# Kernel optimization log

Measured on AMD Instinct MI355X. Metric: run time of the kernel, lower is better.

## Reference

```python
import jax, jax.numpy as jnp
import numpy as np

C = 256        # channels
HEADS = 4
D = C // HEADS # per-head dim
M = 3          # num modalities
EPS = 1e-5
NEG_SLOPE = 0.2  # PyG GATv2 leaky_relu slope


def setup_inputs() -> dict:
    key = jax.random.key(0)
    ks = iter(jax.random.split(key, 40))
    def nrm(shape, s=0.02):
        return jax.random.normal(next(ks), shape, dtype=jnp.float32) * s
    B, H, W = 2, 128, 128
    inp = {}
    for m in range(M):
        inp[f"modal{m}"] = jax.random.normal(next(ks), (B, C, H, W), dtype=jnp.float32)
    # fusion node initializer MLP: Linear-ReLU-Linear
    inp["fn_w1"] = nrm((C, C)); inp["fn_b1"] = jnp.zeros((C,), jnp.float32)
    inp["fn_w2"] = nrm((C, C)); inp["fn_b2"] = jnp.zeros((C,), jnp.float32)
    # two GATv2 layers + layernorms
    for l in range(2):
        inp[f"l{l}_wl"] = nrm((C, C)); inp[f"l{l}_bl"] = jnp.zeros((C,), jnp.float32)
        inp[f"l{l}_wr"] = nrm((C, C)); inp[f"l{l}_br"] = jnp.zeros((C,), jnp.float32)
        inp[f"l{l}_att"] = nrm((HEADS, D), 0.1)
        inp[f"l{l}_bias"] = jnp.zeros((C,), jnp.float32)
        inp[f"ln{l}_g"] = jnp.ones((C,), jnp.float32)
        inp[f"ln{l}_b"] = jnp.zeros((C,), jnp.float32)
    # spatial interaction: conv3x3 (no bias) + BN (eval mode) + ReLU
    inp["conv_w"] = nrm((C, C, 3, 3))
    inp["bn_g"] = jnp.ones((C,), jnp.float32); inp["bn_b"] = jnp.zeros((C,), jnp.float32)
    inp["bn_m"] = jnp.zeros((C,), jnp.float32); inp["bn_v"] = jnp.ones((C,), jnp.float32)
    return inp


def _gatv2(x, wl, bl, wr, br, att, bias):
    # Dense batched GATv2 over P tiny complete graphs (self-loops included,
    # matching PyG GATv2Conv add_self_loops=True default).
    P, N, Cc = x.shape
    xl = (x @ wl + bl).reshape(P, N, HEADS, D)  # source / message features
    xr = (x @ wr + br).reshape(P, N, HEADS, D)  # target features
    e = jax.nn.leaky_relu(xr[:, :, None] + xl[:, None, :], NEG_SLOPE)  # [P,Ni,Nj,H,D]
    scores = jnp.einsum('pijhd,hd->pijh', e, att)
    alpha = jax.nn.softmax(scores, axis=2)  # softmax over source nodes j per target i
    out = jnp.einsum('pijh,pjhd->pihd', alpha, xl)
    return out.reshape(P, N, Cc) + bias


def _layernorm(x, g, b):
    mu = jnp.mean(x, axis=-1, keepdims=True)
    var = jnp.mean((x - mu) ** 2, axis=-1, keepdims=True)
    return (x - mu) * jax.lax.rsqrt(var + EPS) * g + b


def _forward(modal0, modal1, modal2, fn_w1, fn_b1, fn_w2, fn_b2,
             l0_wl, l0_bl, l0_wr, l0_br, l0_att, l0_bias, ln0_g, ln0_b,
             l1_wl, l1_bl, l1_wr, l1_br, l1_att, l1_bias, ln1_g, ln1_b,
             conv_w, bn_g, bn_b, bn_m, bn_v):
    B, _, H, W = modal0.shape
    stacked = jnp.stack([modal0, modal1, modal2], axis=1)        # [B,M,C,H,W]
    modal_nodes = stacked.transpose(0, 3, 4, 1, 2).reshape(-1, M, C)  # [P,M,C]
    mean_feat = jnp.mean(modal_nodes, axis=1, keepdims=True)     # [P,1,C]
    fusion = jax.nn.relu(mean_feat @ fn_w1 + fn_b1) @ fn_w2 + fn_b2
    x = jnp.concatenate([fusion, modal_nodes], axis=1)           # [P,M+1,C]
    for (wl, bl, wr, br, att, bias, g, b) in (
        (l0_wl, l0_bl, l0_wr, l0_br, l0_att, l0_bias, ln0_g, ln0_b),
        (l1_wl, l1_bl, l1_wr, l1_br, l1_att, l1_bias, ln1_g, ln1_b),
    ):
        x = _layernorm(_gatv2(x, wl, bl, wr, br, att, bias) + x, g, b)
    fused = x[:, 0, :].reshape(B, H, W, C).transpose(0, 3, 1, 2)  # [B,C,H,W]
    y = jax.lax.conv_general_dilated(
        fused, conv_w, window_strides=(1, 1), padding='SAME',
        dimension_numbers=('NCHW', 'OIHW', 'NCHW'))
    bc = lambda v: v[None, :, None, None]
    y = (y - bc(bn_m)) * bc(jax.lax.rsqrt(bn_v + EPS)) * bc(bn_g) + bc(bn_b)
    y = jax.nn.relu(y)
    return y + fused


def reference(modal0, modal1, modal2, fn_w1, fn_b1, fn_w2, fn_b2,
              l0_wl, l0_bl, l0_wr, l0_br, l0_att, l0_bias, ln0_g, ln0_b,
              l1_wl, l1_bl, l1_wr, l1_br, l1_att, l1_bias, ln1_g, ln1_b,
              conv_w, bn_g, bn_b, bn_m, bn_v):
    return _forward(modal0, modal1, modal2, fn_w1, fn_b1, fn_w2, fn_b2,
                    l0_wl, l0_bl, l0_wr, l0_br, l0_att, l0_bias, ln0_g, ln0_b,
                    l1_wl, l1_bl, l1_wr, l1_br, l1_att, l1_bias, ln1_g, ln1_b,
                    conv_w, bn_g, bn_b, bn_m, bn_v)
```

## Files before the change

kernel.cpp:

```cpp
#include <hip/hip_runtime.h>


#define Pn 32768
#define PADR 16900

typedef __attribute__((ext_vector_type(8))) short bf16x8;
typedef __attribute__((ext_vector_type(4))) float f32x4;
typedef __attribute__((ext_vector_type(4))) unsigned short u16x4;
typedef __attribute__((ext_vector_type(8))) unsigned short u16x8;
typedef __attribute__((ext_vector_type(2))) unsigned int u32x2;

__device__ __forceinline__ float b2f(short s) {
  unsigned u = ((unsigned)(unsigned short)s) << 16;
  float f;
  __builtin_memcpy(&f, &u, 4);
  return f;
}
__device__ __forceinline__ float asf(unsigned u) {
  float f;
  __builtin_memcpy(&f, &u, 4);
  return f;
}
__device__ __forceinline__ short f2b(float f) {
  unsigned u;
  __builtin_memcpy(&u, &f, 4);
  u += 0x7fffu + ((u >> 16) & 1u);
  return (short)(u >> 16);
}
__device__ __forceinline__ float ldany(const void* p, int i, int bf) {
  return bf ? b2f(((const short*)p)[i]) : ((const float*)p)[i];
}
__device__ __forceinline__ void gload_lds16(const short* g, short* l) {
  __builtin_amdgcn_global_load_lds(
      (const __attribute__((address_space(1))) unsigned int*)g,
      (__attribute__((address_space(3))) unsigned int*)l, 16, 0, 0);
}

__device__ __forceinline__ int xcd_swz(int bid, int nwg) {
  int q = nwg >> 3, r = nwg & 7;
  int x = bid & 7, p = bid >> 3;
  return (x < r ? x * (q + 1) : r * (q + 1) + (x - r) * q) + p;
}

template <int CTRL>
__device__ __forceinline__ float dpp_add(float v) {
  int s;
  __builtin_memcpy(&s, &v, 4);
  int m = __builtin_amdgcn_update_dpp(0, s, CTRL, 0xF, 0xF, false);
  float f;
  __builtin_memcpy(&f, &m, 4);
  return v + f;
}
__device__ __forceinline__ float rsum16(float v) {
  v = dpp_add<0x121>(v);
  v = dpp_add<0x122>(v);
  v = dpp_add<0x124>(v);
  v = dpp_add<0x128>(v);
  return v;
}

__global__ __launch_bounds__(256) void detect_dtype(const void* probe, int* flag) {
  const short* s = (const short*)probe;
  int cnt = 0;
#pragma unroll
  for (int i = 0; i < 8; ++i) {
    short v = s[(threadIdx.x * 8 + i) * 2];
    int e = ((unsigned short)v >> 7) & 0xFF;
    cnt += (e >= 100 && e <= 127) ? 1 : 0;
  }
  __shared__ int tot;
  if (threadIdx.x == 0) tot = 0;
  __syncthreads();
  atomicAdd(&tot, cnt);
  __syncthreads();
  if (threadIdx.x == 0) flag[0] = (tot > 1024) ? 1 : 0;
}

struct P18 { const void* p[18]; };
__global__ __launch_bounds__(256) void prep_params(P18 s, const int* flag, float* pb) {
  int bf = *flag;
  int t = threadIdx.x;
#pragma unroll
  for (int v = 0; v < 18; ++v) pb[v * 256 + t] = ldany(s.p[v], t, bf);
}

__global__ __launch_bounds__(256) void prep_gemm_w(
    const void* w0, const void* w1, const void* w2, const void* w3,
    const void* w4, const void* w5, const int* flag, short* wt) {
  int bf = *flag;
  const void* src;
  switch (blockIdx.y) {
    case 0: src = w0; break;
    case 1: src = w1; break;
    case 2: src = w2; break;
    case 3: src = w3; break;
    case 4: src = w4; break;
    default: src = w5; break;
  }
  int idx = blockIdx.x * 256 + threadIdx.x;
  int ntile = idx >> 12;
  int kt = (idx >> 9) & 7;
  int l = (idx >> 3) & 63;
  int j = idx & 7;
  int r = l & 15, q = l >> 4;
  int n = ntile * 16 + r;
  int k = kt * 32 + q * 8 + j;
  wt[blockIdx.y * 65536 + idx] = f2b(ldany(src, k * 256 + n, bf));
}

__global__ __launch_bounds__(256) void prep_conv_w(const void* cw, const int* flag,
                                                   short* cwt) {
  int bf = *flag;
  int idx = blockIdx.x * 256 + threadIdx.x;
  int tap = idx >> 16;
  int n = (idx >> 8) & 255;
  int k = idx & 255;
  cwt[idx] = f2b(ldany(cw, (n * 256 + k) * 9 + tap, bf));
}

__global__ __launch_bounds__(256) void zero_border(short* rowsPad) {
  int id = blockIdx.x;
  int b = id >= 516;
  int r = id - b * 516;
  int hp, wp;
  if (r < 130)      { hp = 0;       wp = r; }
  else if (r < 260) { hp = 129;     wp = r - 130; }
  else if (r < 388) { hp = r - 259; wp = 0; }
  else              { hp = r - 387; wp = 129; }
  rowsPad[(b * PADR + hp * 130 + wp) * 256 + threadIdx.x] = 0;
}

__global__ __launch_bounds__(256) void gather_chunk(
    const void* m0, const void* m1, const void* m2, const int* flag,
    short* Xc, short* meanc, int sb0) {
  const int bf = *flag;
  const int bx = blockIdx.x;
  const int seg = bx >> 2;
  const int cb = (bx & 3) * 64;
  const int sb = sb0 + seg;
  const int wt = sb & 1, h = (sb >> 1) & 127, b = sb >> 8;
  const int w0 = wt * 64;
  const int lp0 = seg * 64;
  const int t = threadIdx.x;

  __shared__ short tile[3][64][72];
  const void* srcs[3] = {m0, m1, m2};

  const int lsub = t & 7;
#pragma unroll
  for (int pass = 0; pass < 2; ++pass) {
    int c_l = pass * 32 + (t >> 3);
    long long gbase = ((long long)(b * 256 + cb + c_l) * 128 + h) * 128 + w0 + lsub * 8;
#pragma unroll
    for (int m = 0; m < 3; ++m) {
      u16x8 v;
      if (bf) {
        v = *(const u16x8*)((const short*)srcs[m] + gbase);
      } else {
        const float* gp = (const float*)srcs[m] + gbase;
        f32x4 f0 = *(const f32x4*)gp;
        f32x4 f1 = *(const f32x4*)(gp + 4);
#pragma unroll
        for (int k = 0; k < 4; ++k) {
          v[k] = (unsigned short)f2b(f0[k]);
          v[4 + k] = (unsigned short)f2b(f1[k]);
        }
      }
      *(u16x8*)&tile[m][c_l][lsub * 8] = v;
    }
  }
  __syncthreads();

  const int c0 = (t & 7) * 8;
#pragma unroll
  for (int pass = 0; pass < 2; ++pass) {
    int w_l = pass * 32 + (t >> 3);
    float mv[8];
#pragma unroll
    for (int m = 0; m < 3; ++m) {
      u16x8 v;
#pragma unroll
      for (int k = 0; k < 8; ++k) {
        short s = tile[m][c0 + k][w_l];
        v[k] = (unsigned short)s;
        float f = b2f(s);
        mv[k] = (m == 0) ? f : mv[k] + f;
      }
      *(u16x8*)(Xc + (long long)((lp0 + w_l) * 4 + 1 + m) * 256 + cb + c0) = v;
    }
    u16x8 mb;
#pragma unroll
    for (int k = 0; k < 8; ++k)
      mb[k] = (unsigned short)f2b(mv[k] * (1.f / 3.f));
    *(u16x8*)(meanc + (long long)(lp0 + w_l) * 256 + cb + c0) = mb;
  }
}

template <int RELU>
__global__ __launch_bounds__(256, 3) void gemm_tile(
    const short* __restrict__ A, const short* __restrict__ Bf,
    const float* __restrict__ bias, short* __restrict__ out, int ostride) {
  __shared__ short lds[2][4096];
  const int t = threadIdx.x;
  const int l = t & 63, wv = t >> 6;
  const int bid = blockIdx.y * gridDim.x + blockIdx.x;
  const int wg = xcd_swz(bid, gridDim.x * gridDim.y);
  const int n0 = (wg % gridDim.x) * 128;
  const int m0 = (wg / gridDim.x) * 128;
  const int r = l & 15, q = l >> 4;
  const int wm = wv & 1, wn = wv >> 1;

  const short* Bw = Bf + (((n0 >> 4) + wn * 4) << 12) + l * 8;

  f32x4 acc[4][4];
#pragma unroll
  for (int a = 0; a < 4; ++a)
#pragma unroll
    for (int c = 0; c < 4; ++c) acc[a][c] = (f32x4){0.f, 0.f, 0.f, 0.f};

  auto stage = [&](int kt, int bufi) {
    const int k0 = kt * 32;
#pragma unroll
    for (int j = 0; j < 2; ++j) {
      int s0 = j * 256 + wv * 64;
      int row = (s0 + l) >> 2;
      int chs = (l & 3) ^ ((row >> 1) & 3);
      gload_lds16(A + (m0 + row) * 256 + k0 + chs * 8, &lds[bufi][s0 * 8]);
    }
  };

  stage(0, 0);
  __syncthreads();
#pragma unroll
  for (int kt = 0; kt < 8; ++kt) {
    const int cur = kt & 1;
    bf16x8 bfr[4], af[4];
#pragma unroll
    for (int c = 0; c < 4; ++c)
      bfr[c] = *(const bf16x8*)(Bw + (c * 8 + kt) * 512);
#pragma unroll
    for (int a = 0; a < 4; ++a) {
      int R = wm * 64 + a * 16 + r;
      int ch = q ^ ((R >> 1) & 3);
      af[a] = *(const bf16x8*)(&lds[cur][R * 32 + ch * 8]);
    }
    if (kt < 7) stage(kt + 1, cur ^ 1);
#pragma unroll
    for (int a = 0; a < 4; ++a)
#pragma unroll
      for (int c = 0; c < 4; ++c)
        acc[a][c] = __builtin_amdgcn_mfma_f32_16x16x32_bf16(
            af[a], bfr[c], acc[a][c], 0, 0, 0);
    if (kt < 7) __syncthreads();
  }

#pragma unroll
  for (int c = 0; c < 4; ++c) {
    int n = n0 + wn * 64 + c * 16 + r;
    float bs = bias[n];
#pragma unroll
    for (int a = 0; a < 4; ++a)
#pragma unroll
      for (int i = 0; i < 4; ++i) {
        int m = m0 + wm * 64 + a * 16 + q * 4 + i;
        float v = acc[a][c][i] + bs;
        if (RELU) v = fmaxf(v, 0.f);
        out[m * ostride + n] = f2b(v);
      }
  }
}

__global__ __launch_bounds__(256) void attn_ln(
    const short* __restrict__ XLRc,
    const float* __restrict__ att, const float* __restrict__ bias,
    const float* __restrict__ lng, const float* __restrict__ lnb,
    short* __restrict__ Xc, int pOff, short* rowsPad, short* fimgb,
    int writeFused) {
  const int lane = threadIdx.x & 63;
  const int wv = threadIdx.x >> 6;
  const int e = lane & 15;
  const int lp = blockIdx.x * 16 + wv * 4 + (lane >> 4);
  const int pg = pOff + lp;

  float out[4][4][4];
#pragma unroll
  for (int h = 0; h < 4; ++h) {
    float av[4];
#pragma unroll
    for (int k = 0; k < 4; ++k) av[k] = att[h * 64 + e * 4 + k];
    float xlf[4][4], xrf[4][4];
#pragma unroll
    for (int j = 0; j < 4; ++j) {
      const short* rb = XLRc + (lp * 4 + j) * 512 + h * 64 + e * 4;
      u32x2 xl2 = *(const u32x2*)rb;
      u32x2 xr2 = *(const u32x2*)(rb + 256);
      xlf[j][0] = asf(xl2[0] << 16); xlf[j][1] = asf(xl2[0] & 0xffff0000u);
      xlf[j][2] = asf(xl2[1] << 16); xlf[j][3] = asf(xl2[1] & 0xffff0000u);
      xrf[j][0] = asf(xr2[0] << 16); xrf[j][1] = asf(xr2[0] & 0xffff0000u);
      xrf[j][2] = asf(xr2[1] << 16); xrf[j][3] = asf(xr2[1] & 0xffff0000u);
    }
    float rp[4], lp_[4];
#pragma unroll
    for (int j = 0; j < 4; ++j) {
      float r = 0.f, l2 = 0.f;
#pragma unroll
      for (int k = 0; k < 4; ++k) {
        r += xrf[j][k] * av[k];
        l2 += xlf[j][k] * av[k];
      }
      rp[j] = r;
      lp_[j] = l2;
    }
#pragma unroll
    for (int i = 0; i < 4; ++i) {
      float s[4];
#pragma unroll
      for (int j = 0; j < 4; ++j) {
        float acc = 0.f;
#pragma unroll
        for (int k = 0; k < 4; ++k) {
          float t = xrf[i][k] + xlf[j][k];
          acc += __builtin_fabsf(t) * av[k];
        }
        float ap = 0.6f * (rp[i] + lp_[j]) + 0.4f * acc;
        s[j] = rsum16(ap);
      }
      float mx = fmaxf(fmaxf(s[0], s[1]), fmaxf(s[2], s[3]));
      float e0 = __expf(s[0] - mx), e1 = __expf(s[1] - mx);
      float e2 = __expf(s[2] - mx), e3 = __expf(s[3] - mx);
      float inv = __builtin_amdgcn_rcpf(e0 + e1 + e2 + e3);
      float a0 = e0 * inv, a1 = e1 * inv, a2 = e2 * inv, a3 = e3 * inv;
#pragma unroll
      for (int k = 0; k < 4; ++k)
        out[i][h][k] =
            a0 * xlf[0][k] + a1 * xlf[1][k] + a2 * xlf[2][k] + a3 * xlf[3][k];
    }
  }

  float biasf[4][4];
#pragma unroll
  for (int h = 0; h < 4; ++h)
#pragma unroll
    for (int k = 0; k < 4; ++k) biasf[h][k] = bias[h * 64 + e * 4 + k];

#pragma unroll
  for (int i = 0; i < 4; ++i) {
    float y[4][4], sm = 0.f;
#pragma unroll
    for (int h = 0; h < 4; ++h) {
      u32x2 rv2 = *(const u32x2*)(Xc + (lp * 4 + i) * 256 + h * 64 + e * 4);
      float r0 = asf(rv2[0] << 16), r1 = asf(rv2[0] & 0xffff0000u);
      float r2 = asf(rv2[1] << 16), r3 = asf(rv2[1] & 0xffff0000u);
      y[h][0] = out[i][h][0] + biasf[h][0] + r0;
      y[h][1] = out[i][h][1] + biasf[h][1] + r1;
      y[h][2] = out[i][h][2] + biasf[h][2] + r2;
      y[h][3] = out[i][h][3] + biasf[h][3] + r3;
      sm += y[h][0] + y[h][1] + y[h][2] + y[h][3];
    }
    sm = rsum16(sm);
    float mu = sm * (1.f / 256.f);
    float vs = 0.f;
#pragma unroll
    for (int h = 0; h < 4; ++h)
#pragma unroll
      for (int k = 0; k < 4; ++k) {
        float d = y[h][k] - mu;
        vs += d * d;
      }
    vs = rsum16(vs);
    float rs = rsqrtf(vs * (1.f / 256.f) + 1e-5f);
#pragma unroll
    for (int h = 0; h < 4; ++h) {
      float g0 = lng[h * 64 + e * 4 + 0], g1 = lng[h * 64 + e * 4 + 1];
      float g2 = lng[h * 64 + e * 4 + 2], g3 = lng[h * 64 + e * 4 + 3];
      float b0 = lnb[h * 64 + e * 4 + 0], b1 = lnb[h * 64 + e * 4 + 1];
      float b2 = lnb[h * 64 + e * 4 + 2], b3 = lnb[h * 64 + e * 4 + 3];
      u16x4 ov;
      ov[0] = (unsigned short)f2b((y[h][0] - mu) * rs * g0 + b0);
      ov[1] = (unsigned short)f2b((y[h][1] - mu) * rs * g1 + b1);
      ov[2] = (unsigned short)f2b((y[h][2] - mu) * rs * g2 + b2);
      ov[3] = (unsigned short)f2b((y[h][3] - mu) * rs * g3 + b3);
      *(u16x4*)(Xc + (lp * 4 + i) * 256 + h * 64 + e * 4) = ov;
      if (writeFused && i == 0) {
        int w = pg & 127, hh = (pg >> 7) & 127, b = pg >> 14;
        *(u16x4*)(rowsPad + (b * PADR + (hh + 1) * 130 + (w + 1)) * 256 +
                  h * 64 + e * 4) = ov;
#pragma unroll
        for (int k = 0; k < 4; ++k) {
          int c = h * 64 + e * 4 + k;
          fimgb[((b * 256 + c) * 128 + hh) * 128 + w] = (short)ov[k];
        }
      }
    }
  }
}

__global__ __launch_bounds__(256) void conv_tile(
    const short* __restrict__ cwt, const short* __restrict__ rowsPad,
    const short* __restrict__ fimgb, const float* __restrict__ bnp,
    const int* __restrict__ flag, void* __restrict__ outp) {
  __shared__ short lds[2][16384];
  const int bf = *flag;
  const int t = threadIdx.x;
  const int l = t & 63, wv = t >> 6;
  const int bid = blockIdx.y * gridDim.x + blockIdx.x;
  const int wg = xcd_swz(bid, gridDim.x * gridDim.y);
  const int pb = wg % gridDim.x;
  const int bb = pb >> 7, h = pb & 127;
  const int m0 = (wg / gridDim.x) * 128;
  const int r = l & 15, q = l >> 4;
  const int wm = wv & 1, wn = wv >> 1;

  f32x4 acc[4][4];
#pragma unroll
  for (int a = 0; a < 4; ++a)
#pragma unroll
    for (int c = 0; c < 4; ++c) acc[a][c] = (f32x4){0.f, 0.f, 0.f, 0.f};

  auto stage = [&](int stp, int bufi) {
    const int tap = stp >> 2, kt = stp & 3;
    const int ty = (tap >= 6) ? 2 : (tap >= 3 ? 1 : 0);
    const int tx = tap - ty * 3;
    const int prow0 = bb * PADR + (h + ty) * 130 + tx;
    const short* Abase = cwt + tap * 65536;
    const int k0 = kt * 64;
#pragma unroll
    for (int j = 0; j < 4; ++j) {
      int flat = (j * 4 + wv) * 64 + l;
      int row = flat >> 3;
      int cs = (flat & 7) ^ (row & 7);
      gload_lds16(Abase + (m0 + row) * 256 + k0 + cs * 8,
                  &lds[bufi][(j * 4 + wv) * 512]);
      gload_lds16(rowsPad + (prow0 + row) * 256 + k0 + cs * 8,
                  &lds[bufi][8192 + (j * 4 + wv) * 512]);
    }
  };

  stage(0, 0);
  __syncthreads();
  int cur = 0;
  for (int stp = 0; stp < 36; ++stp) {
    bf16x8 af[2][4], bfr[2][4];
#pragma unroll
    for (int kh = 0; kh < 2; ++kh) {
#pragma unroll
      for (int a = 0; a < 4; ++a) {
        int R = wm * 64 + a * 16 + r;
        int s = (kh * 4 + q) ^ (R & 7);
        af[kh][a] = *(const bf16x8*)(&lds[cur][R * 64 + s * 8]);
      }
#pragma unroll
      for (int c = 0; c < 4; ++c) {
        int R = wn * 64 + c * 16 + r;
        int s = (kh * 4 + q) ^ (R & 7);
        bfr[kh][c] = *(const bf16x8*)(&lds[cur][8192 + R * 64 + s * 8]);
      }
    }
    if (stp < 35) stage(stp + 1, cur ^ 1);
#pragma unroll
    for (int kh = 0; kh < 2; ++kh)
#pragma unroll
      for (int a = 0; a < 4; ++a)
#pragma unroll
        for (int c = 0; c < 4; ++c)
          acc[a][c] = __builtin_amdgcn_mfma_f32_16x16x32_bf16(
              af[kh][a], bfr[kh][c], acc[a][c], 0, 0, 0);
    if (stp < 35) { __syncthreads(); cur ^= 1; }
  }

#pragma unroll
  for (int a = 0; a < 4; ++a)
#pragma unroll
    for (int i = 0; i < 4; ++i) {
      int m = m0 + wm * 64 + a * 16 + q * 4 + i;
      float scale = rsqrtf(bnp[768 + m] + 1e-5f) * bnp[m];
      float bmean = bnp[512 + m], bbeta = bnp[256 + m];
      int ib = ((bb * 256 + m) * 128 + h) * 128;
#pragma unroll
      for (int c = 0; c < 4; ++c) {
        int w = wn * 64 + c * 16 + r;
        float v = (acc[a][c][i] - bmean) * scale + bbeta;
        v = fmaxf(v, 0.f);
        int idx = ib + w;
        float res = v + b2f(fimgb[idx]);
        if (bf) ((short*)outp)[idx] = f2b(res);
        else    ((float*)outp)[idx] = res;
      }
    }
}

extern "C" void kernel_launch(void* const* d_in, const int* in_sizes, int n_in,
                              void* d_out, int out_size, void* d_ws, size_t ws_size,
                              hipStream_t stream) {
  const long long baseS = 18033680LL;
  int NCH = 8;
  for (int cand = 2; cand <= 8; cand <<= 1) {
    long long tot = (baseS + (32768LL / cand) * 3072LL) * 2LL;
    if (tot <= (long long)ws_size) { NCH = cand; break; }
  }
  const int CPIX = 32768 / NCH;

  short* ws = (short*)d_ws;
  short* FROWSP = ws;
  short* FIMG   = ws + 8652800;
  short* WT     = ws + 17041408;
  short* CWT    = ws + 17434624;
  float* PB     = (float*)(ws + 18024448);
  int*   FLAG   = (int*)(ws + 18033664);
  short* XLRc   = ws + 18033680;
  short* Xc     = XLRc + (long long)CPIX * 2048;
  short* MEANc  = XLRc;
  short* H1c    = XLRc + (long long)CPIX * 256;

  detect_dtype<<<1, 256, 0, stream>>>(d_in[3], FLAG);

  P18 pp;
  pp.p[0] = d_in[4];   pp.p[1] = d_in[6];
  pp.p[2] = d_in[8];   pp.p[3] = d_in[10];
  pp.p[4] = d_in[11];  pp.p[5] = d_in[12];
  pp.p[6] = d_in[13];  pp.p[7] = d_in[14];
  pp.p[8] = d_in[16];  pp.p[9] = d_in[18];
  pp.p[10] = d_in[19]; pp.p[11] = d_in[20];
  pp.p[12] = d_in[21]; pp.p[13] = d_in[22];
  pp.p[14] = d_in[24]; pp.p[15] = d_in[25];
  pp.p[16] = d_in[26]; pp.p[17] = d_in[27];
  prep_params<<<1, 256, 0, stream>>>(pp, FLAG, PB);

  prep_gemm_w<<<dim3(256, 6), 256, 0, stream>>>(d_in[3], d_in[5], d_in[7],
                                                d_in[9], d_in[15], d_in[17],
                                                FLAG, WT);
  prep_conv_w<<<2304, 256, 0, stream>>>(d_in[23], FLAG, CWT);
  zero_border<<<1032, 256, 0, stream>>>(FROWSP);

  for (int ci = 0; ci < NCH; ++ci) {
    gather_chunk<<<(CPIX / 64) * 4, 256, 0, stream>>>(d_in[0], d_in[1], d_in[2],
                                                      FLAG, Xc, MEANc,
                                                      ci * (CPIX / 64));
    gemm_tile<1><<<dim3(2, CPIX / 128), 256, 0, stream>>>(
        MEANc, WT + 0 * 65536, PB + 0 * 256, H1c, 256);
    gemm_tile<0><<<dim3(2, CPIX / 128), 256, 0, stream>>>(
        H1c, WT + 1 * 65536, PB + 1 * 256, Xc, 1024);
    for (int lyr = 0; lyr < 2; ++lyr) {
      gemm_tile<0><<<dim3(4, 4 * CPIX / 128), 256, 0, stream>>>(
          Xc, WT + (2 + 2 * lyr) * 65536, PB + (2 + 6 * lyr) * 256, XLRc, 512);
      attn_ln<<<CPIX / 16, 256, 0, stream>>>(
          XLRc, PB + (4 + 6 * lyr) * 256, PB + (5 + 6 * lyr) * 256,
          PB + (6 + 6 * lyr) * 256, PB + (7 + 6 * lyr) * 256, Xc, ci * CPIX,
          FROWSP, FIMG, lyr);
    }
  }

  conv_tile<<<dim3(256, 2), 256, 0, stream>>>(CWT, FROWSP, FIMG, PB + 14 * 256,
                                              FLAG, d_out);
}
```

Baseline: 586.9 us.

## Reuse staged input rows across horizontal conv taps and read weights from fragment layout

The conv kernel now stages one padded input row-block (130 rows) per vertical tap and k-quarter, and reuses it for all three horizontal taps by shifting the LDS row index. Weights are pre-permuted into MFMA fragment order so each lane loads its A operand straight from global memory/cache instead of through LDS. This cuts LDS staging traffic and LDS size, allowing four blocks per CU, but drops double buffering. Global weight loads now sit directly in the MFMA loop and may add latency.

```diff
diff --git a/kernel.cpp b/kernel.cpp
--- a/kernel.cpp
+++ b/kernel.cpp
@@ -112,9 +112,14 @@
                                                    short* cwt) {
   int bf = *flag;
   int idx = blockIdx.x * 256 + threadIdx.x;
+  int j = idx & 7;
+  int l = (idx >> 3) & 63;
+  int kt32 = (idx >> 9) & 7;
+  int mt = (idx >> 12) & 15;
   int tap = idx >> 16;
-  int n = (idx >> 8) & 255;
-  int k = idx & 255;
+  int r = l & 15, q = l >> 4;
+  int n = mt * 16 + r;
+  int k = kt32 * 32 + q * 8 + j;
   cwt[idx] = f2b(ldany(cw, (n * 256 + k) * 9 + tap, bf));
 }
 
@@ -395,11 +400,11 @@
   }
 }
 
-__global__ __launch_bounds__(256) void conv_tile(
-    const short* __restrict__ cwt, const short* __restrict__ rowsPad,
+__global__ __launch_bounds__(256, 4) void conv_tile(
+    const short* __restrict__ cwtf, const short* __restrict__ rowsPad,
     const short* __restrict__ fimgb, const float* __restrict__ bnp,
     const int* __restrict__ flag, void* __restrict__ outp) {
-  __shared__ short lds[2][16384];
+  __shared__ short lds[8320];
   const int bf = *flag;
   const int t = threadIdx.x;
   const int l = t & 63, wv = t >> 6;
@@ -410,6 +415,7 @@
   const int m0 = (wg / gridDim.x) * 128;
   const int r = l & 15, q = l >> 4;
   const int wm = wv & 1, wn = wv >> 1;
+  const int mtb = (m0 >> 4) + wm * 4;
 
   f32x4 acc[4][4];
 #pragma unroll
@@ -417,55 +423,53 @@
 #pragma unroll
     for (int c = 0; c < 4; ++c) acc[a][c] = (f32x4){0.f, 0.f, 0.f, 0.f};
 
-  auto stage = [&](int stp, int bufi) {
-    const int tap = stp >> 2, kt = stp & 3;
-    const int ty = (tap >= 6) ? 2 : (tap >= 3 ? 1 : 0);
-    const int tx = tap - ty * 3;
-    const int prow0 = bb * PADR + (h + ty) * 130 + tx;
-    const short* Abase = cwt + tap * 65536;
-    const int k0 = kt * 64;
-#pragma unroll
-    for (int j = 0; j < 4; ++j) {
-      int flat = (j * 4 + wv) * 64 + l;
-      int row = flat >> 3;
-      int cs = (flat & 7) ^ (row & 7);
-      gload_lds16(Abase + (m0 + row) * 256 + k0 + cs * 8,
-                  &lds[bufi][(j * 4 + wv) * 512]);
-      gload_lds16(rowsPad + (prow0 + row) * 256 + k0 + cs * 8,
-                  &lds[bufi][8192 + (j * 4 + wv) * 512]);
-    }
-  };
-
-  stage(0, 0);
-  __syncthreads();
-  int cur = 0;
-  for (int stp = 0; stp < 36; ++stp) {
-    bf16x8 af[2][4], bfr[2][4];
-#pragma unroll
-    for (int kh = 0; kh < 2; ++kh) {
-#pragma unroll
-      for (int a = 0; a < 4; ++a) {
-        int R = wm * 64 + a * 16 + r;
-        int s = (kh * 4 + q) ^ (R & 7);
-        af[kh][a] = *(const bf16x8*)(&lds[cur][R * 64 + s * 8]);
-      }
-#pragma unroll
-      for (int c = 0; c < 4; ++c) {
-        int R = wn * 64 + c * 16 + r;
-        int s = (kh * 4 + q) ^ (R & 7);
-        bfr[kh][c] = *(const bf16x8*)(&lds[cur][8192 + R * 64 + s * 8]);
-      }
-    }
-    if (stp < 35) stage(stp + 1, cur ^ 1);
-#pragma unroll
-    for (int kh = 0; kh < 2; ++kh)
-#pragma unroll
-      for (int a = 0; a < 4; ++a)
-#pragma unroll
-        for (int c = 0; c < 4; ++c)
-          acc[a][c] = __builtin_amdgcn_mfma_f32_16x16x32_bf16(
-              af[kh][a], bfr[kh][c], acc[a][c], 0, 0, 0);
-    if (stp < 35) { __syncthreads(); cur ^= 1; }
+  for (int stp = 0; stp < 12; ++stp) {
+    const int ty = stp >> 2, ktq = stp & 3;
+    const long long rbase =
+        ((long long)(bb * PADR + (h + ty) * 130)) * 256 + ktq * 64;
+    if (stp) __syncthreads();
+#pragma unroll
+    for (int p = 0; p < 4; ++p) {
+      int s0 = p * 256 + wv * 64;
+      int s = s0 + l;
+      int row = s >> 3;
+      int cs = (s & 7) ^ (row & 7);
+      gload_lds16(rowsPad + rbase + row * 256 + cs * 8, &lds[s0 * 8]);
+    }
+    if (wv == 0) {
+      int row = 128 + (l >> 5);
+      int kc = (l >> 2) & 7;
+      int w2 = l & 3;
+      unsigned v;
+      __builtin_memcpy(&v, rowsPad + rbase + row * 256 + kc * 8 + w2 * 2, 4);
+      *(unsigned*)&lds[row * 64 + ((kc ^ (row & 7)) * 8) + w2 * 2] = v;
+    }
+    __syncthreads();
+#pragma unroll
+    for (int tx = 0; tx < 3; ++tx) {
+      const int tap = ty * 3 + tx;
+#pragma unroll
+      for (int kh = 0; kh < 2; ++kh) {
+        const int kt32 = ktq * 2 + kh;
+        bf16x8 af[4], bfr[4];
+#pragma unroll
+        for (int a = 0; a < 4; ++a)
+          af[a] = *(const bf16x8*)(
+              cwtf + (((tap * 16 + mtb + a) * 8 + kt32) * 64 + l) * 8);
+#pragma unroll
+        for (int c = 0; c < 4; ++c) {
+          int R = tx + wn * 64 + c * 16 + r;
+          int s = (kh * 4 + q) ^ (R & 7);
+          bfr[c] = *(const bf16x8*)(&lds[R * 64 + s * 8]);
+        }
+#pragma unroll
+        for (int a = 0; a < 4; ++a)
+#pragma unroll
+          for (int c = 0; c < 4; ++c)
+            acc[a][c] = __builtin_amdgcn_mfma_f32_16x16x32_bf16(
+                af[a], bfr[c], acc[a][c], 0, 0, 0);
+      }
+    }
   }
 
 #pragma unroll
```

Result: slower. 635.2 us (+8.2%).
